# Optimization experiments

Hardware: AMD Instinct MI355X
Metric: run time of the kernel (lower is better)

The kernel has to match this reference:

```python
import jax, jax.numpy as jnp
import numpy as np

N, E = 20000, 160000
NFEAT, NHID, NCLASS = 512, 256, 64


def _unif(key, shape):
    s = 1.0 / np.sqrt(shape[-1])
    return jax.random.uniform(key, shape, jnp.float32, -s, s)


def setup_inputs() -> dict:
    key = jax.random.key(0)
    ks = jax.random.split(key, 16)
    return {
        "x": jax.random.normal(ks[0], (N, NFEAT), jnp.float32),
        "edge_index": jax.random.randint(ks[1], (2, E), 0, N, dtype=jnp.int32).astype(jnp.int64),
        "head": 0,
        # Relation 1 (nfeat -> nfeat)
        "r1_g1": _unif(ks[2], (NFEAT, NFEAT)),
        "r1_g2": _unif(ks[3], (NFEAT, NFEAT)),
        "r1_b1": _unif(ks[4], (NFEAT, NFEAT)),
        "r1_b2": _unif(ks[5], (NFEAT, NFEAT)),
        "r1_m": _unif(ks[6], (1, NFEAT)),
        "gc1_w": _unif(ks[7], (NHID, NFEAT)),   # GCNConv.lin.weight [out,in]
        "gc1_b": jnp.zeros((NHID,), jnp.float32),
        # Relation 2 (nhid -> nhid)
        "r2_g1": _unif(ks[8], (NHID, NHID)),
        "r2_g2": _unif(ks[9], (NHID, NHID)),
        "r2_b1": _unif(ks[10], (NHID, NHID)),
        "r2_b2": _unif(ks[11], (NHID, NHID)),
        "r2_m": _unif(ks[12], (1, NHID)),
        "gc2_w": _unif(ks[13], (NCLASS, NHID)),
        "gc2_b": jnp.zeros((NCLASS,), jnp.float32),
    }


def _scatter_mean(vals, idx, n):
    s = jax.ops.segment_sum(vals, idx, num_segments=n)
    c = jax.ops.segment_sum(jnp.ones(idx.shape, vals.dtype), idx, num_segments=n)
    return s / jnp.clip(c, 1.0)[:, None]


def _relation(ft, nb, g1, g2, b1, b2, m):
    # gamma/beta FiLM-style modulation, then TransE-style translation
    gamma = jax.nn.leaky_relu(ft @ g1.T + nb @ g2.T, 0.2) + 1.0
    beta = jax.nn.leaky_relu(ft @ b1.T + nb @ b2.T, 0.2)
    return ft + (gamma * m + beta) - nb


def _gcn(x, edge_index, w, b):
    # PyG GCNConv with add_self_loops=True, symmetric normalization
    n = x.shape[0]
    h = x @ w.T
    loop = jnp.arange(n, dtype=edge_index.dtype)
    row = jnp.concatenate([edge_index[0], loop])
    col = jnp.concatenate([edge_index[1], loop])
    deg = jax.ops.segment_sum(jnp.ones(col.shape, h.dtype), col, num_segments=n)
    dinv = jnp.where(deg > 0, deg ** -0.5, 0.0)
    norm = dinv[row] * dinv[col]
    out = jax.ops.segment_sum(norm[:, None] * h[row], col, num_segments=n)
    return out + b


def _trans_gcn(x, edge_index, rg1, rg2, rb1, rb2, rm, gw, gb, head):
    row, col = edge_index[0], edge_index[1]
    n = x.shape[0]
    num_nb = jax.ops.segment_sum(jnp.ones(row.shape, x.dtype), row, num_segments=n)
    nb = _scatter_mean(x[col], row, n)
    output = _relation(x, nb, rg1, rg2, rb1, rb2, rm)
    h_k = _gcn(x, edge_index, gw, gb)
    if not head:  # tail branch (ablation=0: h_s = output)
        h_s = output @ gw.T
        h_k = (h_k + h_s) / (num_nb + 1.0)[:, None]
    return h_k, output


def reference(x, edge_index, head, r1_g1, r1_g2, r1_b1, r1_b2, r1_m, gc1_w, gc1_b,
              r2_g1, r2_g2, r2_b1, r2_b2, r2_m, gc2_w, gc2_b):
    x1, out1 = _trans_gcn(x, edge_index, r1_g1, r1_g2, r1_b1, r1_b2, r1_m, gc1_w, gc1_b, head)
    x1 = jax.nn.elu(x1)  # dropout is identity in eval mode
    x2, out2 = _trans_gcn(x1, edge_index, r2_g1, r2_g2, r2_b1, r2_b2, r2_m, gc2_w, gc2_b, head)
    return (x2, jax.nn.log_softmax(x2, axis=1), out1, out2)
```

## Files before the change

kernel.cpp:

```cpp
#include <hip/hip_runtime.h>
#include <hip/hip_bf16.h>
#include <stdint.h>

typedef __bf16 bf16;
typedef __attribute__((ext_vector_type(8))) __bf16 bf16x8;
typedef __attribute__((ext_vector_type(4))) float f32x4;

#define NNODE 20000
#define NEDGE 160000
#define NFEATD 512
#define NHIDD 256
#define NCLSD 64

__device__ __forceinline__ void async_copy16(const bf16* g, bf16* l) {
  __builtin_amdgcn_global_load_lds((__attribute__((address_space(1))) void*)g,
                                   (__attribute__((address_space(3))) void*)l,
                                   16, 0, 0);
}

struct GemmArgs {
  const bf16 *A1, *A2, *W1, *W2, *zpage;
  int ldA, ldW, K1, Ktot, Nvalid, ldC, Nrows, Arows, Wrows;
  bf16* outB;
  float* outF;
  float* outF2;
  const float* mrow;
  const float* Xf;
  const bf16* Xh;
  const bf16* nbm;
  float* outG;
  bf16* outB2;
  const float* agg;
  const bf16* hself;
  int hld;
  const float* dinv;
  const float* bias;
  const float* rnb;
  int elu;
};

template <int MODE>
__global__ __launch_bounds__(256) void gemm_bt(GemmArgs ga) {
  __shared__ bf16 sA[128 * 32];
  __shared__ bf16 sB[128 * 32];
  const int tid = threadIdx.x;
  const int lane = tid & 63;
  const int w = tid >> 6;
  const int wm = w >> 1, wn = w & 1;
  const int bn0 = blockIdx.x * 128;
  const int bm0 = blockIdx.y * 128;
  const int r0 = tid >> 2;
  const int cbv = (tid & 3) << 3;
  const int aoffs = (wm * 64 + (lane & 15)) * 32 + ((lane >> 4) << 3);
  const int boffs = (wn * 64 + (lane & 15)) * 32 + ((lane >> 4) << 3);

  f32x4 acc[4][4] = {};

  const int nseg = (ga.Ktot > ga.K1) ? 2 : 1;
  for (int seg = 0; seg < nseg; seg++) {
    const bf16* As = seg ? ga.A2 : ga.A1;
    const bf16* Ws = seg ? ga.W2 : ga.W1;
    const int rA0 = bm0 + r0;
    const int rW0 = bn0 + r0;
    const bf16* zp = ga.zpage + tid * 8;
    const bf16* pa0 = (rA0 < ga.Arows) ? As + (size_t)rA0 * ga.ldA + cbv : zp;
    const bf16* pa1 = (rA0 + 64 < ga.Arows) ? As + (size_t)(rA0 + 64) * ga.ldA + cbv : zp;
    const bf16* pw0 = (rW0 < ga.Wrows) ? Ws + (size_t)rW0 * ga.ldW + cbv : zp;
    const bf16* pw1 = (rW0 + 64 < ga.Wrows) ? Ws + (size_t)(rW0 + 64) * ga.ldW + cbv : zp;
    const int nit = ga.K1 >> 5;
    for (int it = 0; it < nit; ++it) {
      async_copy16(pa0, sA + tid * 8);
      async_copy16(pa1, sA + (tid + 256) * 8);
      async_copy16(pw0, sB + tid * 8);
      async_copy16(pw1, sB + (tid + 256) * 8);
      __syncthreads();
      bf16x8 af[4], bfv[4];
#pragma unroll
      for (int mi = 0; mi < 4; mi++) af[mi] = *(const bf16x8*)&sA[aoffs + mi * 512];
#pragma unroll
      for (int ni = 0; ni < 4; ni++) bfv[ni] = *(const bf16x8*)&sB[boffs + ni * 512];
#pragma unroll
      for (int mi = 0; mi < 4; mi++)
#pragma unroll
        for (int ni = 0; ni < 4; ni++)
          acc[mi][ni] = __builtin_amdgcn_mfma_f32_16x16x32_bf16(af[mi], bfv[ni], acc[mi][ni], 0, 0, 0);
      __syncthreads();
      pa0 += 32; pa1 += 32; pw0 += 32; pw1 += 32;
    }
  }

  if constexpr (MODE == 0) {
    const int Nv = ga.Nvalid;
#pragma unroll
    for (int mi = 0; mi < 4; mi++) {
      const int rb = bm0 + wm * 64 + mi * 16 + ((lane >> 4) << 2);
#pragma unroll
      for (int ni = 0; ni < 4; ni++) {
        const int c = bn0 + wn * 64 + ni * 16 + (lane & 15);
#pragma unroll
        for (int i = 0; i < 4; i++) {
          const int r = rb + i;
          if (r < ga.Nrows && c < Nv) ga.outB[(size_t)r * ga.ldC + c] = (bf16)acc[mi][ni][i];
        }
      }
    }
  } else if constexpr (MODE == 2) {
    const int Dr = ga.Nvalid;
    const int Lb = ((bn0 + wn * 64) >> 1) + (lane & 15);
#pragma unroll
    for (int mi = 0; mi < 4; mi++) {
      const int rb = bm0 + wm * 64 + mi * 16 + ((lane >> 4) << 2);
#pragma unroll
      for (int p = 0; p < 2; p++) {
        const int L = Lb + p * 16;
        const float mv = ga.mrow[L];
#pragma unroll
        for (int i = 0; i < 4; i++) {
          const int r = rb + i;
          if (r >= ga.Nrows) continue;
          const size_t idx = (size_t)r * Dr + L;
          float vg = acc[mi][2 * p][i];
          float vb = acc[mi][2 * p + 1][i];
          float gamma = (vg > 0.f ? vg : 0.2f * vg) + 1.0f;
          float beta = vb > 0.f ? vb : 0.2f * vb;
          float ft = ga.Xf ? ga.Xf[idx] : (float)ga.Xh[idx];
          float o = ft + gamma * mv + beta - (float)ga.nbm[idx];
          ga.outG[idx] = o;
          ga.outB2[idx] = (bf16)o;
        }
      }
    }
  } else if constexpr (MODE == 3) {
    const int Nv = ga.Nvalid;
#pragma unroll
    for (int mi = 0; mi < 4; mi++) {
      const int rb = bm0 + wm * 64 + mi * 16 + ((lane >> 4) << 2);
#pragma unroll
      for (int ni = 0; ni < 4; ni++) {
        const int c = bn0 + wn * 64 + ni * 16 + (lane & 15);
#pragma unroll
        for (int i = 0; i < 4; i++) {
          const int r = rb + i;
          if (r >= ga.Nrows || c >= Nv) continue;
          const size_t idx = (size_t)r * ga.ldC + c;
          float dv = ga.dinv[r];
          float hs = (float)ga.hself[(size_t)r * ga.hld + c];
          float hv = (ga.agg[idx] + dv * dv * hs + ga.bias[c] + acc[mi][ni][i]) * ga.rnb[r];
          if (ga.elu) hv = hv > 0.f ? hv : expm1f(hv);
          ga.outB[idx] = (bf16)hv;
        }
      }
    }
  } else {
    if (wn == 0) {
#pragma unroll
      for (int mi = 0; mi < 4; mi++) {
        const int rb = bm0 + wm * 64 + mi * 16 + ((lane >> 4) << 2);
#pragma unroll
        for (int i = 0; i < 4; i++) {
          const int r = rb + i;
          const bool ok = r < ga.Nrows;
          float dv = ok ? ga.dinv[r] : 0.f;
          float rn = ok ? ga.rnb[r] : 1.f;
          float hv[4];
#pragma unroll
          for (int ni = 0; ni < 4; ni++) {
            const int c = ni * 16 + (lane & 15);
            float hs = ok ? (float)ga.hself[(size_t)r * ga.hld + c] : 0.f;
            float ag = ok ? ga.agg[(size_t)r * 64 + c] : 0.f;
            hv[ni] = ok ? (ag + dv * dv * hs + ga.bias[c] + acc[mi][ni][i]) * rn : 0.f;
          }
          float mx = fmaxf(fmaxf(hv[0], hv[1]), fmaxf(hv[2], hv[3]));
          mx = fmaxf(mx, __shfl_xor(mx, 1));
          mx = fmaxf(mx, __shfl_xor(mx, 2));
          mx = fmaxf(mx, __shfl_xor(mx, 4));
          mx = fmaxf(mx, __shfl_xor(mx, 8));
          float s = expf(hv[0] - mx) + expf(hv[1] - mx) + expf(hv[2] - mx) + expf(hv[3] - mx);
          s += __shfl_xor(s, 1);
          s += __shfl_xor(s, 2);
          s += __shfl_xor(s, 4);
          s += __shfl_xor(s, 8);
          float ls = logf(s);
          if (ok) {
#pragma unroll
            for (int ni = 0; ni < 4; ni++) {
              const int c = ni * 16 + (lane & 15);
              ga.outF[(size_t)r * 64 + c] = hv[ni];
              ga.outF2[(size_t)r * 64 + c] = hv[ni] - mx - ls;
            }
          }
        }
      }
    }
  }
}

__global__ void cvt_f2b(const float* __restrict__ src, bf16* __restrict__ dst, int n) {
  int i = (blockIdx.x * 256 + threadIdx.x) * 4;
  if (i >= n) return;
  float4 v = *(const float4*)(src + i);
  dst[i + 0] = (bf16)v.x;
  dst[i + 1] = (bf16)v.y;
  dst[i + 2] = (bf16)v.z;
  dst[i + 3] = (bf16)v.w;
}

__global__ void build_rel_w(const float* __restrict__ g1, const float* __restrict__ g2,
                            const float* __restrict__ b1, const float* __restrict__ b2,
                            bf16* __restrict__ dst, int D) {
  int idx = (blockIdx.x * 256 + threadIdx.x) * 4;
  if (idx >= 4 * D * D) return;
  int R = idx / (2 * D), C = idx % (2 * D);
  int q = R >> 5, s = R & 31;
  int sr = q * 16 + (s & 15);
  const float* src = (s < 16) ? ((C < D) ? g1 : g2) : ((C < D) ? b1 : b2);
  int cc = (C < D) ? C : C - D;
  float4 v = *(const float4*)(src + (size_t)sr * D + cc);
  union { bf16 b[4]; uint2 u; } o;
  o.b[0] = (bf16)v.x; o.b[1] = (bf16)v.y; o.b[2] = (bf16)v.z; o.b[3] = (bf16)v.w;
  *(uint2*)(dst + (size_t)R * 2 * D + C) = o.u;
}

__global__ void count_int(const int* __restrict__ ei, int* cr, int* cc, int E) {
  int e = blockIdx.x * 256 + threadIdx.x;
  if (e < E) {
    atomicAdd(&cr[ei[e]], 1);
    atomicAdd(&cc[ei[E + e]], 1);
  }
}

__global__ void scan_excl2(const int* __restrict__ cr, const int* __restrict__ cc,
                           int* __restrict__ rptr, int* __restrict__ cptr,
                           int* __restrict__ curr, int* __restrict__ curc, int n) {
  const int* cnt = blockIdx.x ? cc : cr;
  int* ptr = blockIdx.x ? cptr : rptr;
  int* cur = blockIdx.x ? curc : curr;
  __shared__ int part[256];
  int t = threadIdx.x;
  int chunk = (n + 255) / 256;
  int base = t * chunk;
  int s = 0;
  for (int i = 0; i < chunk; i++) {
    int j = base + i;
    if (j < n) s += cnt[j];
  }
  part[t] = s;
  __syncthreads();
  if (t == 0) {
    int r = 0;
    for (int i = 0; i < 256; i++) { int v = part[i]; part[i] = r; r += v; }
    ptr[n] = r;
  }
  __syncthreads();
  int run = part[t];
  for (int i = 0; i < chunk; i++) {
    int j = base + i;
    if (j < n) {
      ptr[j] = run;
      cur[j] = run;
      run += cnt[j];
    }
  }
}

__global__ void csr_fill(const int* __restrict__ ei, int* cur_r, int* cur_c,
                         int* __restrict__ adj_r, int* __restrict__ adj_c, int E) {
  int e = blockIdx.x * 256 + threadIdx.x;
  if (e >= E) return;
  int row = ei[e], col = ei[E + e];
  int p = atomicAdd(&cur_r[row], 1);
  adj_r[p] = col;
  int q = atomicAdd(&cur_c[col], 1);
  adj_c[q] = row;
}

__global__ void finalize_counts_i(const int* __restrict__ cr, const int* __restrict__ cc,
                                  float* nbscale, float* rnb, float* dinv, int n) {
  int i = blockIdx.x * 256 + threadIdx.x;
  if (i < n) {
    float a = (float)cr[i];
    nbscale[i] = 1.0f / fmaxf(a, 1.0f);
    rnb[i] = 1.0f / (a + 1.0f);
    dinv[i] = rsqrtf((float)cc[i] + 1.0f);
  }
}

__global__ void spmm_nb1(const int* __restrict__ rowptr, const int* __restrict__ adj,
                         const bf16* __restrict__ x, const float* __restrict__ nbscale,
                         bf16* __restrict__ nbp, int n) {
  int r = blockIdx.x * 4 + (threadIdx.x >> 6);
  if (r >= n) return;
  int lane = threadIdx.x & 63;
  int e0 = rowptr[r], e1 = rowptr[r + 1];
  float a[8] = {0.f, 0.f, 0.f, 0.f, 0.f, 0.f, 0.f, 0.f};
  for (int e = e0; e < e1; e++) {
    union { uint4 u; bf16 b[8]; } v;
    v.u = *(const uint4*)(x + (size_t)adj[e] * NFEATD + lane * 8);
#pragma unroll
    for (int j = 0; j < 8; j++) a[j] += (float)v.b[j];
  }
  float s = nbscale[r];
  union { bf16 b[8]; uint4 u; } o;
#pragma unroll
  for (int j = 0; j < 8; j++) o.b[j] = (bf16)(a[j] * s);
  *(uint4*)(nbp + (size_t)r * NFEATD + lane * 8) = o.u;
}

__global__ void spmm_nb2(const int* __restrict__ rowptr, const int* __restrict__ adj,
                         const bf16* __restrict__ x, const float* __restrict__ nbscale,
                         bf16* __restrict__ nbp, int n) {
  int r = blockIdx.x * 4 + (threadIdx.x >> 6);
  if (r >= n) return;
  int lane = threadIdx.x & 63;
  int e0 = rowptr[r], e1 = rowptr[r + 1];
  float a[4] = {0.f, 0.f, 0.f, 0.f};
  for (int e = e0; e < e1; e++) {
    union { uint2 u; bf16 b[4]; } v;
    v.u = *(const uint2*)(x + (size_t)adj[e] * NHIDD + lane * 4);
#pragma unroll
    for (int j = 0; j < 4; j++) a[j] += (float)v.b[j];
  }
  float s = nbscale[r];
  union { bf16 b[4]; uint2 u; } o;
#pragma unroll
  for (int j = 0; j < 4; j++) o.b[j] = (bf16)(a[j] * s);
  *(uint2*)(nbp + (size_t)r * NHIDD + lane * 4) = o.u;
}

__global__ void spmm_gcn256(const int* __restrict__ colptr, const int* __restrict__ adj,
                            const bf16* __restrict__ h, int hld, const float* __restrict__ dinv,
                            float* __restrict__ agg, int n) {
  int c = blockIdx.x * 4 + (threadIdx.x >> 6);
  if (c >= n) return;
  int lane = threadIdx.x & 63;
  int e0 = colptr[c], e1 = colptr[c + 1];
  float a[4] = {0.f, 0.f, 0.f, 0.f};
  for (int e = e0; e < e1; e++) {
    int rr = adj[e];
    float wv = dinv[rr];
    union { uint2 u; bf16 b[4]; } v;
    v.u = *(const uint2*)(h + (size_t)rr * hld + lane * 4);
#pragma unroll
    for (int j = 0; j < 4; j++) a[j] += wv * (float)v.b[j];
  }
  float wc = dinv[c];
  f32x4 o;
#pragma unroll
  for (int j = 0; j < 4; j++) o[j] = a[j] * wc;
  *(f32x4*)(agg + (size_t)c * NHIDD + lane * 4) = o;
}

__global__ void spmm_gcn64(const int* __restrict__ colptr, const int* __restrict__ adj,
                           const bf16* __restrict__ h, int hld, const float* __restrict__ dinv,
                           float* __restrict__ agg, int n) {
  int c = blockIdx.x * 4 + (threadIdx.x >> 6);
  if (c >= n) return;
  int lane = threadIdx.x & 63;
  int e0 = colptr[c], e1 = colptr[c + 1];
  float a = 0.f;
  for (int e = e0; e < e1; e++) {
    int rr = adj[e];
    a += dinv[rr] * (float)h[(size_t)rr * hld + lane];
  }
  agg[(size_t)c * NCLSD + lane] = a * dinv[c];
}

extern "C" void kernel_launch(void* const* d_in, const int* in_sizes, int n_in, void* d_out,
                              int out_size, void* d_ws, size_t ws_size, hipStream_t stream) {
  const float* x = (const float*)d_in[0];
  const int* ei = (const int*)d_in[1];
  const float* r1g1 = (const float*)d_in[3];
  const float* r1g2 = (const float*)d_in[4];
  const float* r1b1 = (const float*)d_in[5];
  const float* r1b2 = (const float*)d_in[6];
  const float* r1m = (const float*)d_in[7];
  const float* gc1w = (const float*)d_in[8];
  const float* gc1b = (const float*)d_in[9];
  const float* r2g1 = (const float*)d_in[10];
  const float* r2g2 = (const float*)d_in[11];
  const float* r2b1 = (const float*)d_in[12];
  const float* r2b2 = (const float*)d_in[13];
  const float* r2m = (const float*)d_in[14];
  const float* gc2w = (const float*)d_in[15];
  const float* gc2b = (const float*)d_in[16];
  float* out = (float*)d_out;

  char* ws = (char*)d_ws;
  size_t off = 0;
  auto alloc = [&](size_t bytes) -> char* {
    char* p = ws + off;
    off = (off + bytes + 511) & ~(size_t)511;
    return p;
  };
  float* nbscale = (float*)alloc((size_t)NNODE * 4);
  float* rnb = (float*)alloc((size_t)NNODE * 4);
  float* dinv = (float*)alloc((size_t)NNODE * 4);
  int* icr = (int*)alloc((size_t)NNODE * 4);
  int* icc = (int*)alloc((size_t)NNODE * 4);
  int* rptr = (int*)alloc((size_t)(NNODE + 1) * 4);
  int* cptr = (int*)alloc((size_t)(NNODE + 1) * 4);
  int* curr = (int*)alloc((size_t)NNODE * 4);
  int* curc = (int*)alloc((size_t)NNODE * 4);
  int* adjr = (int*)alloc((size_t)NEDGE * 4);
  int* adjc = (int*)alloc((size_t)NEDGE * 4);
  bf16* zpage = (bf16*)alloc(8192);
  bf16* Wrel1 = (bf16*)alloc((size_t)1024 * 1024 * 2);
  bf16* Wrel2 = (bf16*)alloc((size_t)512 * 512 * 2);
  bf16* wgc1 = (bf16*)alloc((size_t)NHIDD * NFEATD * 2);
  bf16* wgc2 = (bf16*)alloc((size_t)NCLSD * NHIDD * 2);
  bf16* xb = (bf16*)alloc((size_t)NNODE * NFEATD * 2);
  bf16* nbp1 = (bf16*)alloc((size_t)NNODE * NFEATD * 2);
  bf16* out1b = (bf16*)alloc((size_t)NNODE * NFEATD * 2);
  bf16* h1b = (bf16*)alloc((size_t)NNODE * NHIDD * 2);
  float* agg1 = (float*)alloc((size_t)NNODE * NHIDD * 4);
  bf16* x1b = (bf16*)alloc((size_t)NNODE * NHIDD * 2);
  bf16* nb2p = (bf16*)alloc((size_t)NNODE * NHIDD * 2);
  bf16* out2b = (bf16*)alloc((size_t)NNODE * NHIDD * 2);
  bf16* h2b = (bf16*)alloc((size_t)NNODE * NCLSD * 2);
  float* agg2 = (float*)alloc((size_t)NNODE * NCLSD * 4);

  const size_t OUT1OFF = (size_t)2 * NNODE * NCLSD;
  const size_t OUT2OFF = OUT1OFF + (size_t)NNODE * NFEATD;
  float* out1g = out + OUT1OFF;
  float* out2g = out + OUT2OFF;

  const int MB = (NNODE + 127) / 128;
  const int NW4 = (NNODE + 3) / 4;

  hipMemsetAsync(icr, 0, (size_t)NNODE * 4, stream);
  hipMemsetAsync(icc, 0, (size_t)NNODE * 4, stream);
  hipMemsetAsync(zpage, 0, 8192, stream);
  count_int<<<(NEDGE + 255) / 256, 256, 0, stream>>>(ei, icr, icc, NEDGE);
  scan_excl2<<<2, 256, 0, stream>>>(icr, icc, rptr, cptr, curr, curc, NNODE);
  finalize_counts_i<<<(NNODE + 255) / 256, 256, 0, stream>>>(icr, icc, nbscale, rnb, dinv, NNODE);
  csr_fill<<<(NEDGE + 255) / 256, 256, 0, stream>>>(ei, curr, curc, adjr, adjc, NEDGE);

  cvt_f2b<<<(NNODE * NFEATD / 4 + 255) / 256, 256, 0, stream>>>(x, xb, NNODE * NFEATD);
  cvt_f2b<<<(NHIDD * NFEATD / 4 + 255) / 256, 256, 0, stream>>>(gc1w, wgc1, NHIDD * NFEATD);
  cvt_f2b<<<(NCLSD * NHIDD / 4 + 255) / 256, 256, 0, stream>>>(gc2w, wgc2, NCLSD * NHIDD);
  build_rel_w<<<(4 * 512 * 512 / 4 + 255) / 256, 256, 0, stream>>>(r1g1, r1g2, r1b1, r1b2, Wrel1, 512);
  build_rel_w<<<(4 * 256 * 256 / 4 + 255) / 256, 256, 0, stream>>>(r2g1, r2g2, r2b1, r2b2, Wrel2, 256);

  spmm_nb1<<<NW4, 256, 0, stream>>>(rptr, adjr, xb, nbscale, nbp1, NNODE);

  GemmArgs a;
  auto base = [&](const bf16* A1, const bf16* A2, int ldA, const bf16* W1, const bf16* W2,
                  int ldW, int K1, int Kt, int Nv, int ldC, int Wr) {
    a = GemmArgs{};
    a.A1 = A1; a.A2 = A2; a.W1 = W1; a.W2 = W2; a.zpage = zpage;
    a.ldA = ldA; a.ldW = ldW; a.K1 = K1; a.Ktot = Kt; a.Nvalid = Nv; a.ldC = ldC;
    a.Nrows = NNODE; a.Arows = NNODE; a.Wrows = Wr;
  };

  base(xb, nbp1, NFEATD, Wrel1, Wrel1 + 512, 1024, NFEATD, 2 * NFEATD, NFEATD, NFEATD, 1024);
  a.mrow = r1m; a.Xf = x; a.nbm = nbp1; a.outG = out1g; a.outB2 = out1b;
  gemm_bt<2><<<dim3(8, MB), 256, 0, stream>>>(a);

  base(xb, xb, NFEATD, wgc1, wgc1, NFEATD, NFEATD, NFEATD, NHIDD, NHIDD, NHIDD);
  a.outB = h1b;
  gemm_bt<0><<<dim3(2, MB), 256, 0, stream>>>(a);

  spmm_gcn256<<<NW4, 256, 0, stream>>>(cptr, adjc, h1b, NHIDD, dinv, agg1, NNODE);

  base(out1b, out1b, NFEATD, wgc1, wgc1, NFEATD, NFEATD, NFEATD, NHIDD, NHIDD, NHIDD);
  a.agg = agg1; a.hself = h1b; a.hld = NHIDD; a.dinv = dinv; a.bias = gc1b; a.rnb = rnb;
  a.elu = 1; a.outB = x1b;
  gemm_bt<3><<<dim3(2, MB), 256, 0, stream>>>(a);

  spmm_nb2<<<NW4, 256, 0, stream>>>(rptr, adjr, x1b, nbscale, nb2p, NNODE);

  base(x1b, nb2p, NHIDD, Wrel2, Wrel2 + 256, 512, NHIDD, 2 * NHIDD, NHIDD, NHIDD, 512);
  a.mrow = r2m; a.Xf = nullptr; a.Xh = x1b; a.nbm = nb2p; a.outG = out2g; a.outB2 = out2b;
  gemm_bt<2><<<dim3(4, MB), 256, 0, stream>>>(a);

  base(x1b, x1b, NHIDD, wgc2, wgc2, NHIDD, NHIDD, NHIDD, NCLSD, NCLSD, NCLSD);
  a.outB = h2b;
  gemm_bt<0><<<dim3(1, MB), 256, 0, stream>>>(a);

  spmm_gcn64<<<NW4, 256, 0, stream>>>(cptr, adjc, h2b, NCLSD, dinv, agg2, NNODE);

  base(out2b, out2b, NHIDD, wgc2, wgc2, NHIDD, NHIDD, NHIDD, NCLSD, NCLSD, NCLSD);
  a.agg = agg2; a.hself = h2b; a.hld = NCLSD; a.dinv = dinv; a.bias = gc2b; a.rnb = rnb;
  a.elu = 0; a.outF = out; a.outF2 = out + (size_t)NNODE * NCLSD;
  gemm_bt<4><<<dim3(1, MB), 256, 0, stream>>>(a);
}
```

Measured before the change: 556.5 us.

## Double-buffer GEMM LDS tiles with BK=64, XOR swizzle, and XCD-aware block remap

Rewrites the GEMM main loop to prefetch two K-tiles ahead into double-buffered shared memory with explicit waitcnt and barrier control, so global loads overlap MFMA work. The K tile grows from 32 to 64, and an XOR swizzle is applied to LDS addresses to avoid bank conflicts. Workgroups are remapped so neighbouring tiles land on the same XCD for better L2 reuse, and s_setprio is raised around the MFMA block. LDS use grows fourfold, which may lower occupancy, and the hand-written vmcnt counts must exactly match the eight loads issued per stage.

After: 534.7 us. 1.04x faster.

```diff
diff --git a/kernel.cpp b/kernel.cpp
--- a/kernel.cpp
+++ b/kernel.cpp
@@ -41,51 +41,105 @@
 
 template <int MODE>
 __global__ __launch_bounds__(256) void gemm_bt(GemmArgs ga) {
-  __shared__ bf16 sA[128 * 32];
-  __shared__ bf16 sB[128 * 32];
+  __shared__ bf16 sA[2][128 * 64];
+  __shared__ bf16 sB[2][128 * 64];
   const int tid = threadIdx.x;
   const int lane = tid & 63;
   const int w = tid >> 6;
   const int wm = w >> 1, wn = w & 1;
-  const int bn0 = blockIdx.x * 128;
-  const int bm0 = blockIdx.y * 128;
-  const int r0 = tid >> 2;
-  const int cbv = (tid & 3) << 3;
-  const int aoffs = (wm * 64 + (lane & 15)) * 32 + ((lane >> 4) << 3);
-  const int boffs = (wn * 64 + (lane & 15)) * 32 + ((lane >> 4) << 3);
-
-  f32x4 acc[4][4] = {};
-
-  const int nseg = (ga.Ktot > ga.K1) ? 2 : 1;
-  for (int seg = 0; seg < nseg; seg++) {
+
+  const int gx = gridDim.x;
+  const int nwg = gx * gridDim.y;
+  const int orig = blockIdx.y * gx + blockIdx.x;
+  const int qq = nwg >> 3, rm = nwg & 7;
+  const int xcd = orig & 7, sidx = orig >> 3;
+  const int wg = (xcd < rm ? xcd * (qq + 1) : rm * (qq + 1) + (xcd - rm) * qq) + sidx;
+  const int bn0 = (wg % gx) * 128;
+  const int bm0 = (wg / gx) * 128;
+
+  const int srow = tid >> 3;
+  const int scol = (((tid & 7) ^ (srow & 7)) << 3);
+  const bf16* zp = ga.zpage + tid * 8;
+  int offA[4], offB[4];
+  bool okA[4], okB[4];
+#pragma unroll
+  for (int r = 0; r < 4; r++) {
+    const int ra = bm0 + r * 32 + srow;
+    const int rb = bn0 + r * 32 + srow;
+    okA[r] = ra < ga.Arows;
+    okB[r] = rb < ga.Wrows;
+    offA[r] = ra * ga.ldA + scol;
+    offB[r] = rb * ga.ldW + scol;
+  }
+  const int nt1 = ga.K1 >> 6;
+  const int nt = ga.Ktot >> 6;
+
+  auto stage = [&](int t, int p) {
+    const int seg = t >= nt1;
+    const int koff = (t - (seg ? nt1 : 0)) << 6;
     const bf16* As = seg ? ga.A2 : ga.A1;
     const bf16* Ws = seg ? ga.W2 : ga.W1;
-    const int rA0 = bm0 + r0;
-    const int rW0 = bn0 + r0;
-    const bf16* zp = ga.zpage + tid * 8;
-    const bf16* pa0 = (rA0 < ga.Arows) ? As + (size_t)rA0 * ga.ldA + cbv : zp;
-    const bf16* pa1 = (rA0 + 64 < ga.Arows) ? As + (size_t)(rA0 + 64) * ga.ldA + cbv : zp;
-    const bf16* pw0 = (rW0 < ga.Wrows) ? Ws + (size_t)rW0 * ga.ldW + cbv : zp;
-    const bf16* pw1 = (rW0 + 64 < ga.Wrows) ? Ws + (size_t)(rW0 + 64) * ga.ldW + cbv : zp;
-    const int nit = ga.K1 >> 5;
-    for (int it = 0; it < nit; ++it) {
-      async_copy16(pa0, sA + tid * 8);
-      async_copy16(pa1, sA + (tid + 256) * 8);
-      async_copy16(pw0, sB + tid * 8);
-      async_copy16(pw1, sB + (tid + 256) * 8);
-      __syncthreads();
-      bf16x8 af[4], bfv[4];
-#pragma unroll
-      for (int mi = 0; mi < 4; mi++) af[mi] = *(const bf16x8*)&sA[aoffs + mi * 512];
-#pragma unroll
-      for (int ni = 0; ni < 4; ni++) bfv[ni] = *(const bf16x8*)&sB[boffs + ni * 512];
-#pragma unroll
-      for (int mi = 0; mi < 4; mi++)
-#pragma unroll
-        for (int ni = 0; ni < 4; ni++)
-          acc[mi][ni] = __builtin_amdgcn_mfma_f32_16x16x32_bf16(af[mi], bfv[ni], acc[mi][ni], 0, 0, 0);
-      __syncthreads();
-      pa0 += 32; pa1 += 32; pw0 += 32; pw1 += 32;
+    bf16* dA = &sA[p][tid * 8];
+    bf16* dB = &sB[p][tid * 8];
+#pragma unroll
+    for (int r = 0; r < 4; r++)
+      async_copy16(okA[r] ? As + offA[r] + koff : zp, dA + r * 2048);
+#pragma unroll
+    for (int r = 0; r < 4; r++)
+      async_copy16(okB[r] ? Ws + offB[r] + koff : zp, dB + r * 2048);
+  };
+
+  const int sl = lane >> 4;
+  const int rAb = wm * 64 + (lane & 15);
+  const int rBb = wn * 64 + (lane & 15);
+  const int a7 = rAb & 7, b7 = rBb & 7;
+
+  f32x4 acc[4][4] = {};
+
+  stage(0, 0);
+  stage(1, 1);
+  asm volatile("s_waitcnt vmcnt(8)" ::: "memory");
+  __builtin_amdgcn_s_barrier();
+  asm volatile("" ::: "memory");
+
+  for (int t = 0; t < nt; ++t) {
+    const int p = t & 1;
+    const bf16* pA = &sA[p][0];
+    const bf16* pB = &sB[p][0];
+    bf16x8 af[4][2], bv[4][2];
+#pragma unroll
+    for (int mi = 0; mi < 4; mi++)
+#pragma unroll
+      for (int kk = 0; kk < 2; kk++)
+        af[mi][kk] = *(const bf16x8*)((const char*)pA + (rAb + mi * 16) * 128 +
+                                      ((((kk << 2) + sl) ^ a7) << 4));
+#pragma unroll
+    for (int ni = 0; ni < 4; ni++)
+#pragma unroll
+      for (int kk = 0; kk < 2; kk++)
+        bv[ni][kk] = *(const bf16x8*)((const char*)pB + (rBb + ni * 16) * 128 +
+                                      ((((kk << 2) + sl) ^ b7) << 4));
+    if (t + 2 < nt) {
+      asm volatile("s_waitcnt lgkmcnt(0)" ::: "memory");
+      __builtin_amdgcn_s_barrier();
+      asm volatile("" ::: "memory");
+      stage(t + 2, p);
+    }
+    __builtin_amdgcn_s_setprio(1);
+#pragma unroll
+    for (int mi = 0; mi < 4; mi++)
+#pragma unroll
+      for (int ni = 0; ni < 4; ni++)
+#pragma unroll
+        for (int kk = 0; kk < 2; kk++)
+          acc[mi][ni] =
+              __builtin_amdgcn_mfma_f32_16x16x32_bf16(af[mi][kk], bv[ni][kk], acc[mi][ni], 0, 0, 0);
+    __builtin_amdgcn_s_setprio(0);
+    if (t + 1 < nt) {
+      if (t + 2 < nt) asm volatile("s_waitcnt vmcnt(8)" ::: "memory");
+      else            asm volatile("s_waitcnt vmcnt(0)" ::: "memory");
+      __builtin_amdgcn_s_barrier();
+      asm volatile("" ::: "memory");
     }
   }
 
```
